# Kernel optimization log

Hardware: AMD Instinct MI355X
Metric: run time of the kernel (lower is better)

The kernel has to match this reference:

```python
import jax, jax.numpy as jnp
from jax import lax
import numpy as np

B, S, D, H = 16, 4096, 256, 256


def setup_inputs() -> dict:
    key = jax.random.key(0)
    k1, k2, k3, k4 = jax.random.split(key, 4)
    scale_x = 1.0 / np.sqrt(D)
    scale_h = 1.0 / np.sqrt(H)
    return {
        "inputs": jax.random.normal(k1, (B, S, D), dtype=jnp.float32),
        "state0": jnp.zeros((B, H), dtype=jnp.float32),
        "Wx": jax.random.normal(k2, (D, H), dtype=jnp.float32) * scale_x,
        "Wh": jax.random.normal(k3, (H, H), dtype=jnp.float32) * scale_h,
        "b": jnp.zeros((H,), dtype=jnp.float32),
    }


def reference(inputs, state0, Wx, Wh, b):
    # inputs: [B, S, D] -> time-major [S, B, D] (mirrors inputs.transpose_(0,1))
    x_tm = jnp.transpose(inputs, (1, 0, 2))
    # Precompute the input projection for all timesteps in one GEMM
    x_proj = jnp.einsum("sbd,dh->sbh", x_tm, Wx) + b  # [S, B, H]

    def step(h, xp_t):
        h_new = jnp.tanh(xp_t + h @ Wh)  # cell update; get_output = identity
        return h_new, h_new  # dropout p=0.0 -> identity

    _, outs = lax.scan(step, state0, x_proj)  # outs: [S, B, H]
    return jnp.transpose(outs, (1, 0, 2))  # back to [B, S, H]
```

## Files before the change

### kernel.cpp

```cpp
#include <hip/hip_runtime.h>

#define B_ 16
#define S_ 4096
#define D_ 256
#define H_ 256

typedef _Float16 h2 __attribute__((ext_vector_type(2)));
typedef _Float16 h8 __attribute__((ext_vector_type(8)));
typedef float f4 __attribute__((ext_vector_type(4)));

static __device__ __forceinline__ float fdot2f(h2 a, h2 b, float c) {
    return __builtin_amdgcn_fdot2(a, b, c, false);
}

template <int CTRL>
static __device__ __forceinline__ float dpp_qp(float v) {
    int r = __builtin_amdgcn_update_dpp(0, __float_as_int(v), CTRL, 0xF, 0xF, true);
    return __int_as_float(r);
}
#define DPP_XOR1 0xB1
#define DPP_XOR2 0x4E

static __device__ __forceinline__ void lds_barrier() {
    asm volatile("s_waitcnt lgkmcnt(0)" ::: "memory");
    __builtin_amdgcn_s_barrier();
}

static __device__ __forceinline__ int swz(int i) {
    const int s = i >> 6, r = (i >> 3) & 7, e = i & 7;
    return 64 * s + 8 * ((r + 2 * s) & 7) + e;
}

__global__ __launch_bounds__(256) void xproj_kernel(
    const float* __restrict__ x, const float* __restrict__ Wx,
    const float* __restrict__ bias, float* __restrict__ out)
{
    __shared__ float xs[32 * 256];
    const int tid = threadIdx.x;
    const long long row0 = (long long)blockIdx.x * 32;

    {
        const f4* __restrict__ xg = (const f4*)(x + row0 * D_);
        f4* xsv = (f4*)xs;
        #pragma unroll
        for (int k = 0; k < 8; ++k)
            xsv[tid + k * 256] = xg[tid + k * 256];
    }
    __syncthreads();

    const int j = tid;
    float acc[32];
    const float bj = bias[j];
    #pragma unroll
    for (int r = 0; r < 32; ++r) acc[r] = bj;

    for (int d4 = 0; d4 < D_ / 4; ++d4) {
        const float w0 = Wx[(d4 * 4 + 0) * H_ + j];
        const float w1 = Wx[(d4 * 4 + 1) * H_ + j];
        const float w2 = Wx[(d4 * 4 + 2) * H_ + j];
        const float w3 = Wx[(d4 * 4 + 3) * H_ + j];
        #pragma unroll
        for (int r = 0; r < 32; ++r) {
            f4 xv = *(const f4*)&xs[r * 256 + d4 * 4];
            acc[r] = fmaf(xv.x, w0, acc[r]);
            acc[r] = fmaf(xv.y, w1, acc[r]);
            acc[r] = fmaf(xv.z, w2, acc[r]);
            acc[r] = fmaf(xv.w, w3, acc[r]);
        }
    }
    #pragma unroll
    for (int r = 0; r < 32; ++r)
        out[(row0 + r) * H_ + j] = acc[r];
}

__global__ __launch_bounds__(256, 1) void scan_kernel(
    const float* __restrict__ Wh, const float* __restrict__ state0,
    float* __restrict__ out)
{
    __shared__ __align__(16) _Float16 hbuf[2][H_];
    const int tid = threadIdx.x;
    const int s = tid & 3;
    const int q = tid >> 2;
    const int b = blockIdx.x;
    const bool o1 = (s & 1) != 0;
    const bool o2 = (s & 2) != 0;

    h2 w[4][32];
    #pragma unroll
    for (int jj = 0; jj < 4; ++jj) {
        const int j = 4 * q + jj;
        #pragma unroll
        for (int ii = 0; ii < 32; ++ii) {
            const int i = 64 * s + 2 * ii;
            h2 p;
            p[0] = (_Float16)Wh[(long long)i * H_ + j];
            p[1] = (_Float16)Wh[(long long)(i + 1) * H_ + j];
            w[jj][ii] = p;
        }
    }

    hbuf[0][swz(tid)] = (_Float16)state0[b * H_ + tid];

    float* __restrict__ outb = out + (long long)b * S_ * H_;

    float xr[4];
    #pragma unroll
    for (int k = 0; k < 4; ++k)
        xr[k] = outb[(long long)k * H_ + tid];
    __syncthreads();

    #pragma unroll 4
    for (int st = 0; st < S_; ++st) {
        const int p = st & 1;
        const _Float16* hb = hbuf[p];

        h8 hv[8];
        #pragma unroll
        for (int r = 0; r < 8; ++r)
            hv[r] = *(const h8*)&hb[64 * s + 8 * ((r + 2 * s) & 7)];

        float acc0 = 0.f, acc1 = 0.f, acc2 = 0.f, acc3 = 0.f;
        #pragma unroll
        for (int r = 0; r < 8; ++r) {
            union { h8 v; h2 pr[4]; } u;
            u.v = hv[r];
            #pragma unroll
            for (int m = 0; m < 4; ++m) {
                const int ii = 4 * r + m;
                acc0 = fdot2f(u.pr[m], w[0][ii], acc0);
                acc1 = fdot2f(u.pr[m], w[1][ii], acc1);
                acc2 = fdot2f(u.pr[m], w[2][ii], acc2);
                acc3 = fdot2f(u.pr[m], w[3][ii], acc3);
            }
        }

        float vA = o1 ? acc1 : acc0;
        float vB = o1 ? acc3 : acc2;
        float sA = o1 ? acc0 : acc1;
        float sB = o1 ? acc2 : acc3;
        vA += dpp_qp<DPP_XOR1>(sA);
        vB += dpp_qp<DPP_XOR1>(sB);
        float v   = o2 ? vB : vA;
        float snd = o2 ? vA : vB;
        v += dpp_qp<DPP_XOR2>(snd);

        const float pre = v + xr[st & 3];
        const float e = __builtin_amdgcn_exp2f(pre * 2.8853900817779268f);
        const float hn = fmaf(-2.f, __builtin_amdgcn_rcpf(e + 1.f), 1.f);

        outb[(long long)st * H_ + tid] = hn;
        hbuf[p ^ 1][swz(tid)] = (_Float16)hn;

        const int nt = st + 4;
        xr[st & 3] = (nt < S_) ? outb[(long long)nt * H_ + tid] : 0.f;
        lds_barrier();
    }
}

extern "C" void kernel_launch(void* const* d_in, const int* in_sizes, int n_in,
                              void* d_out, int out_size, void* d_ws, size_t ws_size,
                              hipStream_t stream) {
    const float* x  = (const float*)d_in[0];
    const float* s0 = (const float*)d_in[1];
    const float* Wx = (const float*)d_in[2];
    const float* Wh = (const float*)d_in[3];
    const float* bv = (const float*)d_in[4];
    float* out = (float*)d_out;

    xproj_kernel<<<dim3((B_ * S_) / 32), dim3(256), 0, stream>>>(x, Wx, bv, out);
    scan_kernel<<<dim3(B_), dim3(256), 0, stream>>>(Wh, s0, out);
}
```

Measured before the change: 1.865 ms.

## Repartition recurrent matvec: 8 outputs per thread over 8-lane K-split

Changes the scan kernel's work split from 4 outputs per thread with a 4-way K-split to 8 outputs per thread with an 8-way K-split. Each thread now reads 4 h8 vectors (64 halves) from LDS per step instead of 8, which halves LDS read traffic on the serial critical path. The cost is a third cross-lane reduction stage using DPP row-rotate-by-8. The h-state layout in LDS and the output/x ownership mapping are reworked to match.

```diff
diff --git a/kernel.cpp b/kernel.cpp
--- a/kernel.cpp
+++ b/kernel.cpp
@@ -14,21 +14,22 @@
 }
 
 template <int CTRL>
-static __device__ __forceinline__ float dpp_qp(float v) {
+static __device__ __forceinline__ float dpp_mv(float v) {
     int r = __builtin_amdgcn_update_dpp(0, __float_as_int(v), CTRL, 0xF, 0xF, true);
     return __int_as_float(r);
 }
 #define DPP_XOR1 0xB1
 #define DPP_XOR2 0x4E
+#define DPP_ROR8 0x128
 
 static __device__ __forceinline__ void lds_barrier() {
     asm volatile("s_waitcnt lgkmcnt(0)" ::: "memory");
     __builtin_amdgcn_s_barrier();
 }
 
-static __device__ __forceinline__ int swz(int i) {
-    const int s = i >> 6, r = (i >> 3) & 7, e = i & 7;
-    return 64 * s + 8 * ((r + 2 * s) & 7) + e;
+static __device__ __forceinline__ int hpos(int i) {
+    const int c = i >> 3, e = i & 7;
+    return 8 * ((c >> 2) | ((c & 3) << 3)) + e;
 }
 
 __global__ __launch_bounds__(256) void xproj_kernel(
@@ -78,35 +79,38 @@
     float* __restrict__ out)
 {
     __shared__ __align__(16) _Float16 hbuf[2][H_];
-    const int tid = threadIdx.x;
-    const int s = tid & 3;
-    const int q = tid >> 2;
-    const int b = blockIdx.x;
-    const bool o1 = (s & 1) != 0;
-    const bool o2 = (s & 2) != 0;
+    const int t  = threadIdx.x;
+    const int sl = (t & 3) | ((t >> 1) & 4);
+    const int g  = ((t >> 2) & 1) | ((t >> 4) << 1);
+    const int b  = blockIdx.x;
+    const int j_own = 8 * g + sl;
+    const bool s1 = (sl & 1) != 0, s2 = (sl & 2) != 0, s4 = (sl & 4) != 0;
 
-    h2 w[4][32];
+    h2 w[8][16];
     #pragma unroll
-    for (int jj = 0; jj < 4; ++jj) {
-        const int j = 4 * q + jj;
+    for (int jj = 0; jj < 8; ++jj) {
+        const int j = 8 * g + jj;
         #pragma unroll
-        for (int ii = 0; ii < 32; ++ii) {
-            const int i = 64 * s + 2 * ii;
-            h2 p;
-            p[0] = (_Float16)Wh[(long long)i * H_ + j];
-            p[1] = (_Float16)Wh[(long long)(i + 1) * H_ + j];
-            w[jj][ii] = p;
+        for (int km = 0; km < 16; ++km) {
+            const int i = 32 * sl + 8 * (km >> 2) + 2 * (km & 3);
+            h2 q;
+            q[0] = (_Float16)Wh[(long long)i * H_ + j];
+            q[1] = (_Float16)Wh[(long long)(i + 1) * H_ + j];
+            w[jj][km] = q;
         }
     }
 
-    hbuf[0][swz(tid)] = (_Float16)state0[b * H_ + tid];
+    hbuf[0][hpos(t)] = (_Float16)state0[b * H_ + t];
 
     float* __restrict__ outb = out + (long long)b * S_ * H_;
 
     float xr[4];
     #pragma unroll
     for (int k = 0; k < 4; ++k)
-        xr[k] = outb[(long long)k * H_ + tid];
+        xr[k] = outb[(long long)k * H_ + j_own];
+
+    const int ppos = 8 * ((g >> 2) | ((g & 3) << 3)) + sl;
+    const int rbase = 8 * sl;
     __syncthreads();
 
     #pragma unroll 4
@@ -114,45 +118,60 @@
         const int p = st & 1;
         const _Float16* hb = hbuf[p];
 
-        h8 hv[8];
+        union { h8 v; h2 q[4]; } u0, u1, u2, u3;
+        u0.v = *(const h8*)&hb[rbase];
+        u1.v = *(const h8*)&hb[rbase + 64];
+        u2.v = *(const h8*)&hb[rbase + 128];
+        u3.v = *(const h8*)&hb[rbase + 192];
+
+        float a[8];
         #pragma unroll
-        for (int r = 0; r < 8; ++r)
-            hv[r] = *(const h8*)&hb[64 * s + 8 * ((r + 2 * s) & 7)];
-
-        float acc0 = 0.f, acc1 = 0.f, acc2 = 0.f, acc3 = 0.f;
+        for (int jj = 0; jj < 8; ++jj) a[jj] = 0.f;
         #pragma unroll
-        for (int r = 0; r < 8; ++r) {
-            union { h8 v; h2 pr[4]; } u;
-            u.v = hv[r];
+        for (int m = 0; m < 4; ++m) {
             #pragma unroll
-            for (int m = 0; m < 4; ++m) {
-                const int ii = 4 * r + m;
-                acc0 = fdot2f(u.pr[m], w[0][ii], acc0);
-                acc1 = fdot2f(u.pr[m], w[1][ii], acc1);
-                acc2 = fdot2f(u.pr[m], w[2][ii], acc2);
-                acc3 = fdot2f(u.pr[m], w[3][ii], acc3);
-            }
+            for (int jj = 0; jj < 8; ++jj) a[jj] = fdot2f(u0.q[m], w[jj][m], a[jj]);
+        }
+        #pragma unroll
+        for (int m = 0; m < 4; ++m) {
+            #pragma unroll
+            for (int jj = 0; jj < 8; ++jj) a[jj] = fdot2f(u1.q[m], w[jj][4 + m], a[jj]);
+        }
+        #pragma unroll
+        for (int m = 0; m < 4; ++m) {
+            #pragma unroll
+            for (int jj = 0; jj < 8; ++jj) a[jj] = fdot2f(u2.q[m], w[jj][8 + m], a[jj]);
+        }
+        #pragma unroll
+        for (int m = 0; m < 4; ++m) {
+            #pragma unroll
+            for (int jj = 0; jj < 8; ++jj) a[jj] = fdot2f(u3.q[m], w[jj][12 + m], a[jj]);
         }
 
-        float vA = o1 ? acc1 : acc0;
-        float vB = o1 ? acc3 : acc2;
-        float sA = o1 ? acc0 : acc1;
-        float sB = o1 ? acc2 : acc3;
-        vA += dpp_qp<DPP_XOR1>(sA);
-        vB += dpp_qp<DPP_XOR1>(sB);
-        float v   = o2 ? vB : vA;
-        float snd = o2 ? vA : vB;
-        v += dpp_qp<DPP_XOR2>(snd);
+        float k0 = s1 ? a[1] : a[0], d0 = s1 ? a[0] : a[1];
+        float k1 = s1 ? a[3] : a[2], d1 = s1 ? a[2] : a[3];
+        float k2 = s1 ? a[5] : a[4], d2 = s1 ? a[4] : a[5];
+        float k3 = s1 ? a[7] : a[6], d3 = s1 ? a[6] : a[7];
+        k0 += dpp_mv<DPP_XOR1>(d0);
+        k1 += dpp_mv<DPP_XOR1>(d1);
+        k2 += dpp_mv<DPP_XOR1>(d2);
+        k3 += dpp_mv<DPP_XOR1>(d3);
+        float n0 = s2 ? k1 : k0, e0 = s2 ? k0 : k1;
+        float n1 = s2 ? k3 : k2, e1 = s2 ? k2 : k3;
+        n0 += dpp_mv<DPP_XOR2>(e0);
+        n1 += dpp_mv<DPP_XOR2>(e1);
+        float v  = s4 ? n1 : n0, e2 = s4 ? n0 : n1;
+        v += dpp_mv<DPP_ROR8>(e2);
 
         const float pre = v + xr[st & 3];
         const float e = __builtin_amdgcn_exp2f(pre * 2.8853900817779268f);
         const float hn = fmaf(-2.f, __builtin_amdgcn_rcpf(e + 1.f), 1.f);
 
-        outb[(long long)st * H_ + tid] = hn;
-        hbuf[p ^ 1][swz(tid)] = (_Float16)hn;
+        outb[(long long)st * H_ + j_own] = hn;
+        hbuf[p ^ 1][ppos] = (_Float16)hn;
 
         const int nt = st + 4;
-        xr[st & 3] = (nt < S_) ? outb[(long long)nt * H_ + tid] : 0.f;
+        xr[st & 3] = (nt < S_) ? outb[(long long)nt * H_ + j_own] : 0.f;
         lds_barrier();
     }
 }
```

New measurement: 1.934 ms. +3.7%, slower.

## Compute recurrent matvec with MFMA 16x16x32 instead of fdot2 plus DPP reductions

Applied to the files above, without the earlier changes.

Replaces the per-thread fdot2 dot products and cross-lane DPP reductions in the sequential scan with MFMA f16 instructions. Wh is held in registers as B fragments, and the hidden state is broadcast as the A operand, so all 16 rows compute the same vector. Each lane then picks its own output element from the accumulator. This removes the shuffle reduction and moves the matvec onto the matrix cores. In exchange, 15 of the 16 MFMA rows do redundant work, and the serial per-step latency now depends on MFMA latency.

```diff
diff --git a/kernel.cpp b/kernel.cpp
--- a/kernel.cpp
+++ b/kernel.cpp
@@ -5,30 +5,12 @@
 #define D_ 256
 #define H_ 256
 
-typedef _Float16 h2 __attribute__((ext_vector_type(2)));
-typedef _Float16 h8 __attribute__((ext_vector_type(8)));
+typedef _Float16 h8v __attribute__((ext_vector_type(8)));
 typedef float f4 __attribute__((ext_vector_type(4)));
-
-static __device__ __forceinline__ float fdot2f(h2 a, h2 b, float c) {
-    return __builtin_amdgcn_fdot2(a, b, c, false);
-}
-
-template <int CTRL>
-static __device__ __forceinline__ float dpp_qp(float v) {
-    int r = __builtin_amdgcn_update_dpp(0, __float_as_int(v), CTRL, 0xF, 0xF, true);
-    return __int_as_float(r);
-}
-#define DPP_XOR1 0xB1
-#define DPP_XOR2 0x4E
 
 static __device__ __forceinline__ void lds_barrier() {
     asm volatile("s_waitcnt lgkmcnt(0)" ::: "memory");
     __builtin_amdgcn_s_barrier();
-}
-
-static __device__ __forceinline__ int swz(int i) {
-    const int s = i >> 6, r = (i >> 3) & 7, e = i & 7;
-    return 64 * s + 8 * ((r + 2 * s) & 7) + e;
 }
 
 __global__ __launch_bounds__(256) void xproj_kernel(
@@ -77,82 +59,77 @@
     const float* __restrict__ Wh, const float* __restrict__ state0,
     float* __restrict__ out)
 {
-    __shared__ __align__(16) _Float16 hbuf[2][H_];
+    __shared__ __align__(16) _Float16 h_lds[2][H_];
     const int tid = threadIdx.x;
-    const int s = tid & 3;
-    const int q = tid >> 2;
-    const int b = blockIdx.x;
-    const bool o1 = (s & 1) != 0;
-    const bool o2 = (s & 2) != 0;
+    const int l   = tid & 63;
+    const int wav = tid >> 6;
+    const int lc  = l & 15;
+    const int kg  = l >> 4;
+    const int b   = blockIdx.x;
+    const int j_own = 64 * wav + 16 * kg + lc;
 
-    h2 w[4][32];
+    h8v bf[4][8];
     #pragma unroll
-    for (int jj = 0; jj < 4; ++jj) {
-        const int j = 4 * q + jj;
+    for (int nt = 0; nt < 4; ++nt) {
+        const int j = 64 * wav + 16 * nt + lc;
         #pragma unroll
-        for (int ii = 0; ii < 32; ++ii) {
-            const int i = 64 * s + 2 * ii;
-            h2 p;
-            p[0] = (_Float16)Wh[(long long)i * H_ + j];
-            p[1] = (_Float16)Wh[(long long)(i + 1) * H_ + j];
-            w[jj][ii] = p;
+        for (int ks = 0; ks < 8; ++ks) {
+            #pragma unroll
+            for (int e = 0; e < 8; ++e) {
+                const int k = 32 * ks + 8 * kg + e;
+                bf[nt][ks][e] = (_Float16)Wh[k * H_ + j];
+            }
         }
     }
 
-    hbuf[0][swz(tid)] = (_Float16)state0[b * H_ + tid];
+    h_lds[0][tid] = (_Float16)state0[b * H_ + tid];
 
     float* __restrict__ outb = out + (long long)b * S_ * H_;
 
     float xr[4];
     #pragma unroll
     for (int k = 0; k < 4; ++k)
-        xr[k] = outb[(long long)k * H_ + tid];
+        xr[k] = outb[(long long)k * H_ + j_own];
     __syncthreads();
+
+    const int abase = 8 * kg;
 
     #pragma unroll 4
     for (int st = 0; st < S_; ++st) {
         const int p = st & 1;
-        const _Float16* hb = hbuf[p];
+        const _Float16* hb = h_lds[p];
 
-        h8 hv[8];
+        h8v af[8];
         #pragma unroll
-        for (int r = 0; r < 8; ++r)
-            hv[r] = *(const h8*)&hb[64 * s + 8 * ((r + 2 * s) & 7)];
+        for (int ks = 0; ks < 8; ++ks)
+            af[ks] = *(const h8v*)&hb[32 * ks + abase];
 
-        float acc0 = 0.f, acc1 = 0.f, acc2 = 0.f, acc3 = 0.f;
+        f4 acc0 = {0.f, 0.f, 0.f, 0.f};
+        f4 acc1 = {0.f, 0.f, 0.f, 0.f};
+        f4 acc2 = {0.f, 0.f, 0.f, 0.f};
+        f4 acc3 = {0.f, 0.f, 0.f, 0.f};
         #pragma unroll
-        for (int r = 0; r < 8; ++r) {
-            union { h8 v; h2 pr[4]; } u;
-            u.v = hv[r];
-            #pragma unroll
-            for (int m = 0; m < 4; ++m) {
-                const int ii = 4 * r + m;
-                acc0 = fdot2f(u.pr[m], w[0][ii], acc0);
-                acc1 = fdot2f(u.pr[m], w[1][ii], acc1);
-                acc2 = fdot2f(u.pr[m], w[2][ii], acc2);
-                acc3 = fdot2f(u.pr[m], w[3][ii], acc3);
-            }
+        for (int ks = 0; ks < 8; ++ks) {
+            acc0 = __builtin_amdgcn_mfma_f32_16x16x32_f16(af[ks], bf[0][ks], acc0, 0, 0, 0);
+            acc1 = __builtin_amdgcn_mfma_f32_16x16x32_f16(af[ks], bf[1][ks], acc1, 0, 0, 0);
+            acc2 = __builtin_amdgcn_mfma_f32_16x16x32_f16(af[ks], bf[2][ks], acc2, 0, 0, 0);
+            acc3 = __builtin_amdgcn_mfma_f32_16x16x32_f16(af[ks], bf[3][ks], acc3, 0, 0, 0);
         }
 
-        float vA = o1 ? acc1 : acc0;
-        float vB = o1 ? acc3 : acc2;
-        float sA = o1 ? acc0 : acc1;
-        float sB = o1 ? acc2 : acc3;
-        vA += dpp_qp<DPP_XOR1>(sA);
-        vB += dpp_qp<DPP_XOR1>(sB);
-        float v   = o2 ? vB : vA;
-        float snd = o2 ? vA : vB;
-        v += dpp_qp<DPP_XOR2>(snd);
+        float v = acc0[0];
+        v = (kg == 1) ? acc1[0] : v;
+        v = (kg == 2) ? acc2[0] : v;
+        v = (kg == 3) ? acc3[0] : v;
 
         const float pre = v + xr[st & 3];
         const float e = __builtin_amdgcn_exp2f(pre * 2.8853900817779268f);
         const float hn = fmaf(-2.f, __builtin_amdgcn_rcpf(e + 1.f), 1.f);
 
-        outb[(long long)st * H_ + tid] = hn;
-        hbuf[p ^ 1][swz(tid)] = (_Float16)hn;
+        outb[(long long)st * H_ + j_own] = hn;
+        h_lds[p ^ 1][j_own] = (_Float16)hn;
 
-        const int nt = st + 4;
-        xr[st & 3] = (nt < S_) ? outb[(long long)nt * H_ + tid] : 0.f;
+        const int nt4 = st + 4;
+        xr[st & 3] = (nt4 < S_) ? outb[(long long)nt4 * H_ + j_own] : 0.f;
         lds_barrier();
     }
 }
```

New measurement: 1.919 ms. 2.9% more time.

## Rewrite input projection GEMM with fp16 MFMA and register-resident Wx tiles

Applied to the files above, without the earlier changes.

Replaces the scalar fp32 FMA input-projection kernel with one that uses 16x16x32 fp16 MFMA instructions. Each block keeps its Wx slice in registers as fp16 and streams 256 rows of x through LDS in 16-row chunks, prefetching the next chunk into registers. The goal is to cut the GEMM's compute time. In exchange it lowers the precision of x and Wx to fp16 and launches only 256 blocks.

```diff
diff --git a/kernel.cpp b/kernel.cpp
--- a/kernel.cpp
+++ b/kernel.cpp
@@ -6,7 +6,9 @@
 #define H_ 256
 
 typedef _Float16 h2 __attribute__((ext_vector_type(2)));
+typedef _Float16 h4 __attribute__((ext_vector_type(4)));
 typedef _Float16 h8 __attribute__((ext_vector_type(8)));
+typedef _Float16 h8v __attribute__((ext_vector_type(8)));
 typedef float f4 __attribute__((ext_vector_type(4)));
 
 static __device__ __forceinline__ float fdot2f(h2 a, h2 b, float c) {
@@ -31,46 +33,83 @@
     return 64 * s + 8 * ((r + 2 * s) & 7) + e;
 }
 
-__global__ __launch_bounds__(256) void xproj_kernel(
+__global__ __launch_bounds__(256, 1) void xproj_kernel(
     const float* __restrict__ x, const float* __restrict__ Wx,
     const float* __restrict__ bias, float* __restrict__ out)
 {
-    __shared__ float xs[32 * 256];
+    __shared__ __align__(16) _Float16 xs[16 * 272];
     const int tid = threadIdx.x;
-    const long long row0 = (long long)blockIdx.x * 32;
-
-    {
-        const f4* __restrict__ xg = (const f4*)(x + row0 * D_);
-        f4* xsv = (f4*)xs;
-        #pragma unroll
-        for (int k = 0; k < 8; ++k)
-            xsv[tid + k * 256] = xg[tid + k * 256];
-    }
-    __syncthreads();
-
-    const int j = tid;
-    float acc[32];
-    const float bj = bias[j];
-    #pragma unroll
-    for (int r = 0; r < 32; ++r) acc[r] = bj;
-
-    for (int d4 = 0; d4 < D_ / 4; ++d4) {
-        const float w0 = Wx[(d4 * 4 + 0) * H_ + j];
-        const float w1 = Wx[(d4 * 4 + 1) * H_ + j];
-        const float w2 = Wx[(d4 * 4 + 2) * H_ + j];
-        const float w3 = Wx[(d4 * 4 + 3) * H_ + j];
-        #pragma unroll
-        for (int r = 0; r < 32; ++r) {
-            f4 xv = *(const f4*)&xs[r * 256 + d4 * 4];
-            acc[r] = fmaf(xv.x, w0, acc[r]);
-            acc[r] = fmaf(xv.y, w1, acc[r]);
-            acc[r] = fmaf(xv.z, w2, acc[r]);
-            acc[r] = fmaf(xv.w, w3, acc[r]);
-        }
-    }
-    #pragma unroll
-    for (int r = 0; r < 32; ++r)
-        out[(row0 + r) * H_ + j] = acc[r];
+    const int l   = tid & 63;
+    const int wav = tid >> 6;
+    const int lc  = l & 15;
+    const int kg  = l >> 4;
+    const long long row0 = (long long)blockIdx.x * 256;
+
+    h8v bf[4][8];
+    #pragma unroll
+    for (int nt = 0; nt < 4; ++nt) {
+        const int j = 64 * wav + 16 * nt + lc;
+        #pragma unroll
+        for (int ks = 0; ks < 8; ++ks) {
+            #pragma unroll
+            for (int e = 0; e < 8; ++e)
+                bf[nt][ks][e] = (_Float16)Wx[(32 * ks + 8 * kg + e) * H_ + j];
+        }
+    }
+    float bvv[4];
+    #pragma unroll
+    for (int nt = 0; nt < 4; ++nt)
+        bvv[nt] = bias[64 * wav + 16 * nt + lc];
+
+    f4 pre[4];
+    #pragma unroll
+    for (int k4 = 0; k4 < 4; ++k4)
+        pre[k4] = *(const f4*)&x[(row0 + wav + 4 * k4) * D_ + 4 * l];
+
+    for (int it = 0; it < 16; ++it) {
+        const long long r0 = row0 + it * 16;
+
+        __syncthreads();
+        #pragma unroll
+        for (int k4 = 0; k4 < 4; ++k4) {
+            h4 hv;
+            hv[0] = (_Float16)pre[k4].x;
+            hv[1] = (_Float16)pre[k4].y;
+            hv[2] = (_Float16)pre[k4].z;
+            hv[3] = (_Float16)pre[k4].w;
+            *(h4*)&xs[(wav + 4 * k4) * 272 + 4 * l] = hv;
+        }
+        __syncthreads();
+
+        if (it + 1 < 16) {
+            const long long rn = row0 + (it + 1) * 16;
+            #pragma unroll
+            for (int k4 = 0; k4 < 4; ++k4)
+                pre[k4] = *(const f4*)&x[(rn + wav + 4 * k4) * D_ + 4 * l];
+        }
+
+        f4 acc[4];
+        #pragma unroll
+        for (int nt = 0; nt < 4; ++nt)
+            acc[nt] = (f4){0.f, 0.f, 0.f, 0.f};
+
+        #pragma unroll
+        for (int ks = 0; ks < 8; ++ks) {
+            h8v af = *(const h8v*)&xs[lc * 272 + 32 * ks + 8 * kg];
+            acc[0] = __builtin_amdgcn_mfma_f32_16x16x32_f16(af, bf[0][ks], acc[0], 0, 0, 0);
+            acc[1] = __builtin_amdgcn_mfma_f32_16x16x32_f16(af, bf[1][ks], acc[1], 0, 0, 0);
+            acc[2] = __builtin_amdgcn_mfma_f32_16x16x32_f16(af, bf[2][ks], acc[2], 0, 0, 0);
+            acc[3] = __builtin_amdgcn_mfma_f32_16x16x32_f16(af, bf[3][ks], acc[3], 0, 0, 0);
+        }
+
+        #pragma unroll
+        for (int nt = 0; nt < 4; ++nt) {
+            const int j = 64 * wav + 16 * nt + lc;
+            #pragma unroll
+            for (int r = 0; r < 4; ++r)
+                out[(r0 + 4 * kg + r) * H_ + j] = acc[nt][r] + bvv[nt];
+        }
+    }
 }
 
 __global__ __launch_bounds__(256, 1) void scan_kernel(
@@ -167,6 +206,6 @@
     const float* bv = (const float*)d_in[4];
     float* out = (float*)d_out;
 
-    xproj_kernel<<<dim3((B_ * S_) / 32), dim3(256), 0, stream>>>(x, Wx, bv, out);
+    xproj_kernel<<<dim3((B_ * S_) / 256), dim3(256), 0, stream>>>(x, Wx, bv, out);
     scan_kernel<<<dim3(B_), dim3(256), 0, stream>>>(Wh, s0, out);
 }
```

Result: faster. 1.704 ms (median of 2 runs) (-8.6%).
